# Kernel optimization log

Measured on AMD Instinct MI355X. Metric: run time of the kernel, lower is better.

## Reference

```python
import jax, jax.numpy as jnp
import numpy as np

N = 50000
E = 250000
IN = 256
H = 4
D = 64  # h_feats // n_heads
C = 153


def setup_inputs() -> dict:
    key = jax.random.key(0)
    ks = jax.random.split(key, 32)
    def nrm(k, shape, scale=0.05):
        return jax.random.normal(k, shape, dtype=jnp.float32) * scale
    inp = {
        'x': nrm(ks[0], (N, IN), 1.0),
        'edge_index_a': jax.random.randint(ks[1], (2, E), 0, N, dtype=jnp.int32),
        'edge_index_b': jax.random.randint(ks[2], (2, E), 0, N, dtype=jnp.int32),
    }
    i = 3
    for layer in (0, 1):
        for et in ('a', 'b'):
            inp[f'W{layer}{et}'] = nrm(ks[i], (IN if layer == 0 else H * D, H * D)); i += 1
            inp[f'asrc{layer}{et}'] = nrm(ks[i], (H, D)); i += 1
            inp[f'adst{layer}{et}'] = nrm(ks[i], (H, D)); i += 1
            inp[f'b{layer}{et}'] = nrm(ks[i], (H * D,)); i += 1
    inp['Wout'] = nrm(ks[i], (H * D, C)); i += 1
    inp['bout'] = nrm(ks[i], (C,))
    return inp


def gat_conv(x, edge_index, W, a_src, a_dst, b):
    # PyG GATConv: shared linear, per-edge attention, dst-segmented softmax
    h = (x @ W).reshape(N, H, D)                 # [N, H, D]
    s_src = jnp.sum(h * a_src, axis=-1)          # [N, H]
    s_dst = jnp.sum(h * a_dst, axis=-1)          # [N, H]
    src, dst = edge_index[0], edge_index[1]
    e = jax.nn.leaky_relu(s_src[src] + s_dst[dst], negative_slope=0.2)  # [E, H]
    m = jax.ops.segment_max(e, dst, num_segments=N)                     # [N, H]
    m = jnp.where(jnp.isfinite(m), m, 0.0)       # isolated nodes -> 0
    p = jnp.exp(e - m[dst])                      # [E, H]
    z = jax.ops.segment_sum(p, dst, num_segments=N)
    alpha = p / (z[dst] + 1e-16)                 # [E, H]
    out = jax.ops.segment_sum(h[src] * alpha[:, :, None], dst, num_segments=N)
    return out.reshape(N, H * D) + b


def reference(x, edge_index_a, edge_index_b,
              W0a, asrc0a, adst0a, b0a, W0b, asrc0b, adst0b, b0b,
              W1a, asrc1a, adst1a, b1a, W1b, asrc1b, adst1b, b1b,
              Wout, bout):
    # layer 0: HeteroConv sums outputs of per-etype GATConvs
    h = gat_conv(x, edge_index_a, W0a, asrc0a, adst0a, b0a) + \
        gat_conv(x, edge_index_b, W0b, asrc0b, adst0b, b0b)
    h = jax.nn.leaky_relu(h, negative_slope=0.01)  # F.leaky_relu default; dropout is identity in eval
    # layer 1 (no activation after last layer)
    h = gat_conv(h, edge_index_a, W1a, asrc1a, adst1a, b1a) + \
        gat_conv(h, edge_index_b, W1b, asrc1b, adst1b, b1b)
    return h @ Wout + bout
```

## Files before the change

kernel.cpp:

```cpp
#include <hip/hip_runtime.h>
#include <math.h>

#define N_NODES 50000
#define E_EDGES 250000
#define HD 256
#define NH 4
#define DH 64
#define NC 153
#define KDIM 256
#define HD2 512

__device__ __forceinline__ unsigned short f2bf(float f) {
    unsigned u = __float_as_uint(f);
    u = u + 0x7FFFu + ((u >> 16) & 1u);
    return (unsigned short)(u >> 16);
}
__device__ __forceinline__ float bf2f(unsigned short b) {
    return __uint_as_float(((unsigned)b) << 16);
}

typedef __attribute__((ext_vector_type(8))) short bf16x8;
typedef __attribute__((ext_vector_type(4))) float f32x4;

template<int NCB, bool SCORES>
__global__ __launch_bounds__(256) void gemm_k256(
        const unsigned short* __restrict__ A, const unsigned short* __restrict__ BT,
        float* __restrict__ Cf, unsigned short* __restrict__ Cbf,
        const float* __restrict__ bias,
        const float* __restrict__ as_a, const float* __restrict__ ad_a,
        const float* __restrict__ as_b, const float* __restrict__ ad_b,
        float* __restrict__ ssrc8, float* __restrict__ sdst8,
        int M, int Ncols) {
    __shared__ unsigned short Bs[64 * 256];
    const int tid = threadIdx.x;
    const int lane = tid & 63;
    const int wave = tid >> 6;
    const int quad = lane >> 4;
    const int l16 = lane & 15;

    const int nwg = gridDim.x;
    const int wg = blockIdx.x;
    const int x = wg & 7, ii = wg >> 3;
    const int q = nwg >> 3, r = nwg & 7;
    const int logical = (x < r ? x * (q + 1) : r * (q + 1) + (x - r) * q) + ii;
    const int cb = logical % NCB;
    const int rb = logical / NCB;
    const int row0 = rb * 256 + wave * 64;
    const int col0 = cb * 64;

    #pragma unroll
    for (int j = 0; j < 8; j++) {
        const int c = tid + 256 * j;
        const int rr = c >> 5;
        const int kb = (c & 31) << 4;
        const uint4 v = *(const uint4*)((const char*)BT +
                            (size_t)(col0 + rr) * 512 + kb);
        *(uint4*)((char*)Bs + rr * 512 + (kb ^ ((rr & 7) << 4))) = v;
    }
    __syncthreads();

    f32x4 acc[4][4];
    #pragma unroll
    for (int i = 0; i < 4; i++)
        #pragma unroll
        for (int j = 0; j < 4; j++) acc[i][j] = (f32x4)0.f;

    size_t a_off[4];
    #pragma unroll
    for (int mt = 0; mt < 4; mt++) {
        int gr = row0 + mt * 16 + l16;
        if (gr >= M) gr = M - 1;
        a_off[mt] = (size_t)gr * KDIM + quad * 8;
    }
    const char* Bsc = (const char*)Bs;
    const int bbase = l16 * 512 + ((quad * 16) ^ ((l16 & 7) << 4));

    bf16x8 a_buf[4][4];
    bf16x8 b_cur[4], b_nxt[4];
    #pragma unroll
    for (int s = 0; s < 3; s++)
        #pragma unroll
        for (int mt = 0; mt < 4; mt++)
            a_buf[s][mt] = *(const bf16x8*)&A[a_off[mt] + s * 32];
    #pragma unroll
    for (int nt = 0; nt < 4; nt++)
        b_cur[nt] = *(const bf16x8*)(Bsc + nt * 16 * 512 + bbase);

    #pragma unroll
    for (int kk = 0; kk < 8; kk++) {
        if (kk + 3 < 8) {
            #pragma unroll
            for (int mt = 0; mt < 4; mt++)
                a_buf[(kk + 3) & 3][mt] =
                    *(const bf16x8*)&A[a_off[mt] + (kk + 3) * 32];
        }
        if (kk < 7) {
            #pragma unroll
            for (int nt = 0; nt < 4; nt++)
                b_nxt[nt] = *(const bf16x8*)(Bsc + nt * 16 * 512 +
                                (bbase ^ ((kk + 1) * 64)));
        }
        #pragma unroll
        for (int mt = 0; mt < 4; mt++)
            #pragma unroll
            for (int nt = 0; nt < 4; nt++)
                acc[mt][nt] = __builtin_amdgcn_mfma_f32_16x16x32_bf16(
                                  a_buf[kk & 3][mt], b_cur[nt], acc[mt][nt], 0, 0, 0);
        #pragma unroll
        for (int nt = 0; nt < 4; nt++) b_cur[nt] = b_nxt[nt];
    }

    if constexpr (SCORES) {
        const float* as_p = (cb < 4) ? as_a : as_b;
        const float* ad_p = (cb < 4) ? ad_a : ad_b;
        const int hd = (cb & 3) * 64;
        float asv[4], adv[4];
        #pragma unroll
        for (int nt = 0; nt < 4; nt++) {
            asv[nt] = as_p[hd + nt * 16 + l16];
            adv[nt] = ad_p[hd + nt * 16 + l16];
        }
        #pragma unroll
        for (int mt = 0; mt < 4; mt++) {
            #pragma unroll
            for (int rr = 0; rr < 4; rr++) {
                float ps = acc[mt][0][rr] * asv[0] + acc[mt][1][rr] * asv[1]
                         + acc[mt][2][rr] * asv[2] + acc[mt][3][rr] * asv[3];
                float pd = acc[mt][0][rr] * adv[0] + acc[mt][1][rr] * adv[1]
                         + acc[mt][2][rr] * adv[2] + acc[mt][3][rr] * adv[3];
                #pragma unroll
                for (int off = 1; off < 16; off <<= 1) {
                    ps += __shfl_xor(ps, off);
                    pd += __shfl_xor(pd, off);
                }
                const int m = row0 + mt * 16 + quad * 4 + rr;
                if (l16 == 0 && m < M) {
                    ssrc8[m * 8 + cb] = ps;
                    sdst8[m * 8 + cb] = pd;
                }
            }
        }

        __syncthreads();
        char* myC = (char*)Bs + wave * 8192;
        #pragma unroll
        for (int mt = 0; mt < 4; mt++)
            #pragma unroll
            for (int nt = 0; nt < 4; nt++)
                #pragma unroll
                for (int rr = 0; rr < 4; rr++)
                    *(unsigned short*)(myC + (mt * 16 + quad * 4 + rr) * 128 +
                                       (nt * 16 + l16) * 2) = f2bf(acc[mt][nt][rr]);
        #pragma unroll
        for (int it = 0; it < 8; it++) {
            const int chunk = it * 64 + lane;
            const int lr = chunk >> 3;
            const int cbyte = (chunk & 7) * 16;
            const uint4 v = *(const uint4*)(myC + lr * 128 + cbyte);
            const int m = row0 + lr;
            if (m < M)
                *(uint4*)((char*)Cbf + ((size_t)m * Ncols + col0) * 2 + cbyte) = v;
        }
    } else {
        #pragma unroll
        for (int mt = 0; mt < 4; mt++) {
            #pragma unroll
            for (int nt = 0; nt < 4; nt++) {
                const int n = col0 + nt * 16 + l16;
                if (n >= Ncols) continue;
                const float bv = bias ? bias[n] : 0.f;
                #pragma unroll
                for (int rr = 0; rr < 4; rr++) {
                    const int m = row0 + mt * 16 + quad * 4 + rr;
                    if (m < M) Cf[(size_t)m * Ncols + n] = acc[mt][nt][rr] + bv;
                }
            }
        }
    }
}

__global__ __launch_bounds__(256) void convert_bf16_kernel(
        const float* __restrict__ in, unsigned short* __restrict__ out, int n) {
    const int i = (blockIdx.x * 256 + threadIdx.x) * 4;
    if (i + 3 < n) {
        const float4 v = *(const float4*)&in[i];
        ushort4 o;
        o.x = f2bf(v.x); o.y = f2bf(v.y); o.z = f2bf(v.z); o.w = f2bf(v.w);
        *(ushort4*)&out[i] = o;
    } else {
        for (int j = i; j < n; j++) out[j] = f2bf(in[j]);
    }
}

__global__ __launch_bounds__(256) void wt2_kernel(
        const float* __restrict__ Wa, const float* __restrict__ Wb,
        unsigned short* __restrict__ Wt) {
    const int idx = blockIdx.x * 256 + threadIdx.x;
    const int n = idx >> 8, k = idx & 255;
    Wt[idx] = (n < HD) ? f2bf(Wa[(size_t)k * HD + n])
                       : f2bf(Wb[(size_t)k * HD + (n - HD)]);
}

__global__ __launch_bounds__(256) void wt_kernel(
        const float* __restrict__ W, unsigned short* __restrict__ Wt, int Nc) {
    const int idx = blockIdx.x * 256 + threadIdx.x;
    const int n = idx >> 8, k = idx & 255;
    Wt[idx] = (n < Nc) ? f2bf(W[(size_t)k * Nc + n]) : (unsigned short)0;
}

__global__ __launch_bounds__(256) void zero_int_kernel(int* __restrict__ p, int n) {
    const int i = blockIdx.x * 256 + threadIdx.x;
    if (i < n) p[i] = 0;
}

__global__ __launch_bounds__(256) void hist2_kernel(
        const int* __restrict__ ei_a, const int* __restrict__ ei_b,
        int* __restrict__ deg) {
    const int t = blockIdx.x * 256 + threadIdx.x;
    if (t < E_EDGES)          atomicAdd(&deg[ei_a[E_EDGES + t]], 1);
    else if (t < 2 * E_EDGES) atomicAdd(&deg[N_NODES + ei_b[t]], 1);
}

__global__ __launch_bounds__(1024) void scan_local_kernel(
        const int* __restrict__ deg, int* __restrict__ excl,
        int* __restrict__ bsums, int n) {
    __shared__ int wsum[16];
    const int i = blockIdx.x * 1024 + threadIdx.x;
    const int lane = threadIdx.x & 63;
    const int wid = threadIdx.x >> 6;
    const int v = (i < n) ? deg[i] : 0;
    int s = v;
    #pragma unroll
    for (int off = 1; off < 64; off <<= 1) {
        const int t = __shfl_up(s, off);
        if (lane >= off) s += t;
    }
    if (lane == 63) wsum[wid] = s;
    __syncthreads();
    if (wid == 0) {
        int wv = (lane < 16) ? wsum[lane] : 0;
        #pragma unroll
        for (int off = 1; off < 16; off <<= 1) {
            const int t = __shfl_up(wv, off);
            if (lane >= off) wv += t;
        }
        if (lane < 16) wsum[lane] = wv;
    }
    __syncthreads();
    const int woff = (wid > 0) ? wsum[wid - 1] : 0;
    if (i < n) excl[i] = s - v + woff;
    if (threadIdx.x == 1023) bsums[blockIdx.x] = wsum[15];
}

__global__ __launch_bounds__(64) void scan_bsums_kernel(
        int* __restrict__ bsums, int nb) {
    const int lane = threadIdx.x;
    const int b0 = (lane < nb) ? bsums[lane] : 0;
    const int b1 = (64 + lane < nb) ? bsums[64 + lane] : 0;
    int s0 = b0, s1 = b1;
    #pragma unroll
    for (int off = 1; off < 64; off <<= 1) {
        const int t0 = __shfl_up(s0, off);
        const int t1 = __shfl_up(s1, off);
        if (lane >= off) { s0 += t0; s1 += t1; }
    }
    const int tot0 = __shfl(s0, 63);
    bsums[lane] = s0 - b0;
    bsums[64 + lane] = tot0 + s1 - b1;
}

__global__ __launch_bounds__(256) void scan_add2_kernel(
        const int* __restrict__ excl, const int* __restrict__ bsums,
        int* __restrict__ rp_a, int* __restrict__ rp_b,
        int* __restrict__ cursor, int n2) {
    const int i = blockIdx.x * 256 + threadIdx.x;
    if (i >= n2) return;
    const int v = excl[i] + bsums[i >> 10];
    if (i < N_NODES) { rp_a[i] = v; cursor[i] = v; }
    else { const int w = v - E_EDGES; rp_b[i - N_NODES] = w; cursor[i] = w; }
    if (i == 0) { rp_a[N_NODES] = E_EDGES; rp_b[N_NODES] = E_EDGES; }
}

__global__ __launch_bounds__(256) void scatter2_kernel(
        const int* __restrict__ ei_a, const int* __restrict__ ei_b,
        int* __restrict__ cursor,
        int* __restrict__ cs_a, int* __restrict__ cs_b) {
    const int t = blockIdx.x * 256 + threadIdx.x;
    if (t < E_EDGES) {
        const int src = ei_a[t], dst = ei_a[E_EDGES + t];
        cs_a[atomicAdd(&cursor[dst], 1)] = src;
    } else if (t < 2 * E_EDGES) {
        const int src = ei_b[t - E_EDGES], dst = ei_b[t];
        cs_b[atomicAdd(&cursor[N_NODES + dst], 1)] = src;
    }
}

__global__ __launch_bounds__(256) void aggregate_both_kernel(
        const int* __restrict__ rp_a, const int* __restrict__ cs_a,
        const int* __restrict__ rp_b, const int* __restrict__ cs_b,
        const unsigned short* __restrict__ h_ab,
        const float* __restrict__ ssrc8, const float* __restrict__ sdst8,
        const float* __restrict__ b1, const float* __restrict__ b2,
        unsigned short* __restrict__ out_bf, int do_leaky) {
    const int node = blockIdx.x * 4 + (threadIdx.x >> 6);
    const int lane = threadIdx.x & 63;
    if (node >= N_NODES) return;
    const int hh = lane >> 4;
    const int l16 = lane & 15;
    const int c4 = lane * 4;

    float4 a = make_float4(0.f, 0.f, 0.f, 0.f);

    #pragma unroll
    for (int et = 0; et < 2; et++) {
        const int* rp = et ? rp_b : rp_a;
        const int* cs = et ? cs_b : cs_a;
        const size_t hoff = et ? (size_t)HD : 0;
        const int r8 = et * 4 + hh;
        const float sdv = sdst8[node * 8 + r8];
        const int beg = rp[node], end = rp[node + 1];

        float mm = -INFINITY, z = 0.f;
        for (int c = beg; c < end; c += 16) {
            const int e = c + l16;
            float s = -INFINITY;
            if (e < end) {
                s = ssrc8[cs[e] * 8 + r8] + sdv;
                s = (s >= 0.f) ? s : 0.2f * s;
            }
            float mx = s;
            #pragma unroll
            for (int off = 1; off < 16; off <<= 1)
                mx = fmaxf(mx, __shfl_xor(mx, off));
            const float mn = fmaxf(mm, mx);
            float ee = (e < end) ? expf(s - mn) : 0.f;
            #pragma unroll
            for (int off = 1; off < 16; off <<= 1)
                ee += __shfl_xor(ee, off);
            z = z * expf(mm - mn) + ee;
            mm = mn;
        }
        const float zz = 1.f / (z + 1e-16f);

        int e = beg;
        for (; e + 3 < end; e += 4) {
            const int s0 = cs[e + 0], s1 = cs[e + 1],
                      s2 = cs[e + 2], s3 = cs[e + 3];
            float v0 = ssrc8[s0 * 8 + r8] + sdv; v0 = (v0 >= 0.f) ? v0 : 0.2f * v0;
            float v1 = ssrc8[s1 * 8 + r8] + sdv; v1 = (v1 >= 0.f) ? v1 : 0.2f * v1;
            float v2 = ssrc8[s2 * 8 + r8] + sdv; v2 = (v2 >= 0.f) ? v2 : 0.2f * v2;
            float v3 = ssrc8[s3 * 8 + r8] + sdv; v3 = (v3 >= 0.f) ? v3 : 0.2f * v3;
            const float al0 = expf(v0 - mm) * zz;
            const float al1 = expf(v1 - mm) * zz;
            const float al2 = expf(v2 - mm) * zz;
            const float al3 = expf(v3 - mm) * zz;
            const ushort4 h0 = *(const ushort4*)&h_ab[(size_t)s0 * HD2 + hoff + c4];
            const ushort4 h1 = *(const ushort4*)&h_ab[(size_t)s1 * HD2 + hoff + c4];
            const ushort4 h2 = *(const ushort4*)&h_ab[(size_t)s2 * HD2 + hoff + c4];
            const ushort4 h3 = *(const ushort4*)&h_ab[(size_t)s3 * HD2 + hoff + c4];
            a.x = fmaf(al0, bf2f(h0.x), a.x); a.y = fmaf(al0, bf2f(h0.y), a.y);
            a.z = fmaf(al0, bf2f(h0.z), a.z); a.w = fmaf(al0, bf2f(h0.w), a.w);
            a.x = fmaf(al1, bf2f(h1.x), a.x); a.y = fmaf(al1, bf2f(h1.y), a.y);
            a.z = fmaf(al1, bf2f(h1.z), a.z); a.w = fmaf(al1, bf2f(h1.w), a.w);
            a.x = fmaf(al2, bf2f(h2.x), a.x); a.y = fmaf(al2, bf2f(h2.y), a.y);
            a.z = fmaf(al2, bf2f(h2.z), a.z); a.w = fmaf(al2, bf2f(h2.w), a.w);
            a.x = fmaf(al3, bf2f(h3.x), a.x); a.y = fmaf(al3, bf2f(h3.y), a.y);
            a.z = fmaf(al3, bf2f(h3.z), a.z); a.w = fmaf(al3, bf2f(h3.w), a.w);
        }
        for (; e < end; e++) {
            const int src = cs[e];
            float v0 = ssrc8[src * 8 + r8] + sdv; v0 = (v0 >= 0.f) ? v0 : 0.2f * v0;
            const float al = expf(v0 - mm) * zz;
            const ushort4 hv = *(const ushort4*)&h_ab[(size_t)src * HD2 + hoff + c4];
            a.x = fmaf(al, bf2f(hv.x), a.x);
            a.y = fmaf(al, bf2f(hv.y), a.y);
            a.z = fmaf(al, bf2f(hv.z), a.z);
            a.w = fmaf(al, bf2f(hv.w), a.w);
        }
    }

    const float4 bv1 = *(const float4*)&b1[c4];
    const float4 bv2 = *(const float4*)&b2[c4];
    float4 v;
    v.x = a.x + bv1.x + bv2.x;
    v.y = a.y + bv1.y + bv2.y;
    v.z = a.z + bv1.z + bv2.z;
    v.w = a.w + bv1.w + bv2.w;
    if (do_leaky) {
        v.x = (v.x >= 0.f) ? v.x : 0.01f * v.x;
        v.y = (v.y >= 0.f) ? v.y : 0.01f * v.y;
        v.z = (v.z >= 0.f) ? v.z : 0.01f * v.z;
        v.w = (v.w >= 0.f) ? v.w : 0.01f * v.w;
    }
    ushort4 o;
    o.x = f2bf(v.x); o.y = f2bf(v.y); o.z = f2bf(v.z); o.w = f2bf(v.w);
    *(ushort4*)&out_bf[(size_t)node * HD + c4] = o;
}

#define N_ROWBLK ((N_NODES + 255) / 256)

static void run_layer(const unsigned short* a_bf,
                      const int* rp_a, const int* cs_a,
                      const int* rp_b, const int* cs_b,
                      const float* Wa, const float* Wb,
                      const float* as_a, const float* ad_a,
                      const float* as_b, const float* ad_b,
                      const float* b1, const float* b2,
                      unsigned short* Wt2, unsigned short* h_ab,
                      float* ssrc8, float* sdst8,
                      unsigned short* out_bf, int do_leaky,
                      hipStream_t stream) {
    wt2_kernel<<<HD2, 256, 0, stream>>>(Wa, Wb, Wt2);
    gemm_k256<8, true><<<N_ROWBLK * 8, 256, 0, stream>>>(
        a_bf, Wt2, nullptr, h_ab, nullptr,
        as_a, ad_a, as_b, ad_b, ssrc8, sdst8, N_NODES, HD2);
    aggregate_both_kernel<<<(N_NODES + 3) / 4, 256, 0, stream>>>(
        rp_a, cs_a, rp_b, cs_b, h_ab, ssrc8, sdst8,
        b1, b2, out_bf, do_leaky);
}

extern "C" void kernel_launch(void* const* d_in, const int* in_sizes, int n_in,
                              void* d_out, int out_size, void* d_ws, size_t ws_size,
                              hipStream_t stream) {
    const float* x    = (const float*)d_in[0];
    const int*   ei_a = (const int*)d_in[1];
    const int*   ei_b = (const int*)d_in[2];
    const float* W0a = (const float*)d_in[3];
    const float* as0a = (const float*)d_in[4];
    const float* ad0a = (const float*)d_in[5];
    const float* b0a = (const float*)d_in[6];
    const float* W0b = (const float*)d_in[7];
    const float* as0b = (const float*)d_in[8];
    const float* ad0b = (const float*)d_in[9];
    const float* b0b = (const float*)d_in[10];
    const float* W1a = (const float*)d_in[11];
    const float* as1a = (const float*)d_in[12];
    const float* ad1a = (const float*)d_in[13];
    const float* b1a = (const float*)d_in[14];
    const float* W1b = (const float*)d_in[15];
    const float* as1b = (const float*)d_in[16];
    const float* ad1b = (const float*)d_in[17];
    const float* b1b = (const float*)d_in[18];
    const float* Wout = (const float*)d_in[19];
    const float* bout = (const float*)d_in[20];
    float* out = (float*)d_out;

    unsigned short* h_ab  = (unsigned short*)d_ws;
    unsigned short* bf_in = h_ab + (size_t)N_NODES * HD2;
    unsigned short* Wt2   = bf_in + (size_t)N_NODES * HD;
    float* ssrc8  = (float*)(Wt2 + (size_t)HD2 * KDIM);
    float* sdst8  = ssrc8 + (size_t)N_NODES * 8;
    int*   ibase  = (int*)(sdst8 + (size_t)N_NODES * 8);
    int* deg     = ibase;
    int* cursor  = deg + 2 * N_NODES;
    int* rp_a    = cursor + 2 * N_NODES;
    int* cs_a    = rp_a + N_NODES + 1;
    int* rp_b    = cs_a + E_EDGES;
    int* cs_b    = rp_b + N_NODES + 1;
    int* excl    = cs_b + E_EDGES;
    int* bsums   = excl + 2 * N_NODES;

    const size_t NF = (size_t)N_NODES * HD;
    const int nf4_blocks = (int)((NF / 4 + 255) / 256);
    const int n2 = 2 * N_NODES;
    const int sb = (n2 + 1023) / 1024;

    zero_int_kernel<<<(n2 + 255) / 256, 256, 0, stream>>>(deg, n2);
    hist2_kernel<<<(2 * E_EDGES + 255) / 256, 256, 0, stream>>>(ei_a, ei_b, deg);
    scan_local_kernel<<<sb, 1024, 0, stream>>>(deg, excl, bsums, n2);
    scan_bsums_kernel<<<1, 64, 0, stream>>>(bsums, sb);
    scan_add2_kernel<<<(n2 + 255) / 256, 256, 0, stream>>>(
        excl, bsums, rp_a, rp_b, cursor, n2);
    scatter2_kernel<<<(2 * E_EDGES + 255) / 256, 256, 0, stream>>>(
        ei_a, ei_b, cursor, cs_a, cs_b);

    convert_bf16_kernel<<<nf4_blocks, 256, 0, stream>>>(x, bf_in, (int)NF);
    run_layer(bf_in, rp_a, cs_a, rp_b, cs_b, W0a, W0b,
              as0a, ad0a, as0b, ad0b, b0a, b0b, Wt2, h_ab,
              ssrc8, sdst8, bf_in, 1, stream);

    run_layer(bf_in, rp_a, cs_a, rp_b, cs_b, W1a, W1b,
              as1a, ad1a, as1b, ad1b, b1a, b1b, Wt2, h_ab,
              ssrc8, sdst8, bf_in, 0, stream);

    wt_kernel<<<KDIM, 256, 0, stream>>>(Wout, Wt2, NC);
    gemm_k256<3, false><<<N_ROWBLK * 3, 256, 0, stream>>>(
        bf_in, Wt2, out, nullptr, bout,
        nullptr, nullptr, nullptr, nullptr, nullptr, nullptr, N_NODES, NC);
}
```

Measured before the change: 435.2 us.

## Fuse softmax and aggregation into single-pass online softmax with shuffled edges

Replaces the two-pass attention aggregation (first pass computing max and normalizer, second pass recomputing scores and gathering features) with a single online-softmax pass. Each lane computes one edge's score per 16-edge chunk, and the source index and weight are broadcast via shuffles to accumulate features with rescaling. This removes the second read of column indices and source scores and the duplicate exp work. In exchange it adds per-chunk rescale multiplies and shuffles, and the feature loads depend on the chunk's max reduction, which may serialize latency for low-degree nodes.

```diff
diff --git a/kernel.cpp b/kernel.cpp
--- a/kernel.cpp
+++ b/kernel.cpp
@@ -320,63 +320,65 @@
         const float sdv = sdst8[node * 8 + r8];
         const int beg = rp[node], end = rp[node + 1];
 
-        float mm = -INFINITY, z = 0.f;
+        float m = -INFINITY, z = 0.f;
+        float4 t = make_float4(0.f, 0.f, 0.f, 0.f);
+
         for (int c = beg; c < end; c += 16) {
             const int e = c + l16;
+            const bool valid = (e < end);
+            const int srci = valid ? cs[e] : 0;
             float s = -INFINITY;
-            if (e < end) {
-                s = ssrc8[cs[e] * 8 + r8] + sdv;
+            if (valid) {
+                s = ssrc8[srci * 8 + r8] + sdv;
                 s = (s >= 0.f) ? s : 0.2f * s;
             }
             float mx = s;
             #pragma unroll
             for (int off = 1; off < 16; off <<= 1)
                 mx = fmaxf(mx, __shfl_xor(mx, off));
-            const float mn = fmaxf(mm, mx);
-            float ee = (e < end) ? expf(s - mn) : 0.f;
+            const float mn = fmaxf(m, mx);
+            const float sc = expf(m - mn);
+            t.x *= sc; t.y *= sc; t.z *= sc; t.w *= sc;
+            z *= sc;
+            m = mn;
+            const float p = valid ? expf(s - m) : 0.f;
+            float ps = p;
             #pragma unroll
             for (int off = 1; off < 16; off <<= 1)
-                ee += __shfl_xor(ee, off);
-            z = z * expf(mm - mn) + ee;
-            mm = mn;
+                ps += __shfl_xor(ps, off);
+            z += ps;
+
+            if (c + 16 <= end) {
+                #pragma unroll
+                for (int j = 0; j < 16; j++) {
+                    const int sj = __shfl(srci, hh * 16 + j);
+                    const float aj = __shfl(p, hh * 16 + j);
+                    const ushort4 hv =
+                        *(const ushort4*)&h_ab[(size_t)sj * HD2 + hoff + c4];
+                    t.x = fmaf(aj, bf2f(hv.x), t.x);
+                    t.y = fmaf(aj, bf2f(hv.y), t.y);
+                    t.z = fmaf(aj, bf2f(hv.z), t.z);
+                    t.w = fmaf(aj, bf2f(hv.w), t.w);
+                }
+            } else {
+                const int nl = end - c;
+                for (int j = 0; j < nl; j++) {
+                    const int sj = __shfl(srci, hh * 16 + j);
+                    const float aj = __shfl(p, hh * 16 + j);
+                    const ushort4 hv =
+                        *(const ushort4*)&h_ab[(size_t)sj * HD2 + hoff + c4];
+                    t.x = fmaf(aj, bf2f(hv.x), t.x);
+                    t.y = fmaf(aj, bf2f(hv.y), t.y);
+                    t.z = fmaf(aj, bf2f(hv.z), t.z);
+                    t.w = fmaf(aj, bf2f(hv.w), t.w);
+                }
+            }
         }
         const float zz = 1.f / (z + 1e-16f);
-
-        int e = beg;
-        for (; e + 3 < end; e += 4) {
-            const int s0 = cs[e + 0], s1 = cs[e + 1],
-                      s2 = cs[e + 2], s3 = cs[e + 3];
-            float v0 = ssrc8[s0 * 8 + r8] + sdv; v0 = (v0 >= 0.f) ? v0 : 0.2f * v0;
-            float v1 = ssrc8[s1 * 8 + r8] + sdv; v1 = (v1 >= 0.f) ? v1 : 0.2f * v1;
-            float v2 = ssrc8[s2 * 8 + r8] + sdv; v2 = (v2 >= 0.f) ? v2 : 0.2f * v2;
-            float v3 = ssrc8[s3 * 8 + r8] + sdv; v3 = (v3 >= 0.f) ? v3 : 0.2f * v3;
-            const float al0 = expf(v0 - mm) * zz;
-            const float al1 = expf(v1 - mm) * zz;
-            const float al2 = expf(v2 - mm) * zz;
-            const float al3 = expf(v3 - mm) * zz;
-            const ushort4 h0 = *(const ushort4*)&h_ab[(size_t)s0 * HD2 + hoff + c4];
-            const ushort4 h1 = *(const ushort4*)&h_ab[(size_t)s1 * HD2 + hoff + c4];
-            const ushort4 h2 = *(const ushort4*)&h_ab[(size_t)s2 * HD2 + hoff + c4];
-            const ushort4 h3 = *(const ushort4*)&h_ab[(size_t)s3 * HD2 + hoff + c4];
-            a.x = fmaf(al0, bf2f(h0.x), a.x); a.y = fmaf(al0, bf2f(h0.y), a.y);
-            a.z = fmaf(al0, bf2f(h0.z), a.z); a.w = fmaf(al0, bf2f(h0.w), a.w);
-            a.x = fmaf(al1, bf2f(h1.x), a.x); a.y = fmaf(al1, bf2f(h1.y), a.y);
-            a.z = fmaf(al1, bf2f(h1.z), a.z); a.w = fmaf(al1, bf2f(h1.w), a.w);
-            a.x = fmaf(al2, bf2f(h2.x), a.x); a.y = fmaf(al2, bf2f(h2.y), a.y);
-            a.z = fmaf(al2, bf2f(h2.z), a.z); a.w = fmaf(al2, bf2f(h2.w), a.w);
-            a.x = fmaf(al3, bf2f(h3.x), a.x); a.y = fmaf(al3, bf2f(h3.y), a.y);
-            a.z = fmaf(al3, bf2f(h3.z), a.z); a.w = fmaf(al3, bf2f(h3.w), a.w);
-        }
-        for (; e < end; e++) {
-            const int src = cs[e];
-            float v0 = ssrc8[src * 8 + r8] + sdv; v0 = (v0 >= 0.f) ? v0 : 0.2f * v0;
-            const float al = expf(v0 - mm) * zz;
-            const ushort4 hv = *(const ushort4*)&h_ab[(size_t)src * HD2 + hoff + c4];
-            a.x = fmaf(al, bf2f(hv.x), a.x);
-            a.y = fmaf(al, bf2f(hv.y), a.y);
-            a.z = fmaf(al, bf2f(hv.z), a.z);
-            a.w = fmaf(al, bf2f(hv.w), a.w);
-        }
+        a.x = fmaf(t.x, zz, a.x);
+        a.y = fmaf(t.y, zz, a.y);
+        a.z = fmaf(t.z, zz, a.z);
+        a.w = fmaf(t.w, zz, a.w);
     }
 
     const float4 bv1 = *(const float4*)&b1[c4];
```

Result: slower. 493.1 us (+13.3%).
